# Performance work log

Hardware: AMD Instinct MI355X
Metric: run time of the kernel (lower is better)

## Reference

```python
import jax, jax.numpy as jnp
import numpy as np

PROJ_DIM = 8192
INPUT_DIM = 512
THRESH = 1e-08


def _signed_sqrt(x):
    return jnp.sign(x) * jnp.sqrt(jnp.abs(x))


def _make_sketch_matrix(key, input_dim, proj_dim):
    kh, ks = jax.random.split(key)
    h = jax.random.randint(kh, (input_dim,), 0, proj_dim)
    s = jnp.sign(jax.random.uniform(ks, (input_dim,), minval=-1.0, maxval=1.0)).astype(jnp.float32)
    M = jnp.zeros((input_dim, proj_dim), dtype=jnp.float32)
    return M.at[jnp.arange(input_dim), h].set(s)


def setup_inputs() -> dict:
    key = jax.random.key(0)
    kx, k1, k2 = jax.random.split(key, 3)
    x = jax.random.normal(kx, (32, 14, 14, INPUT_DIM), dtype=jnp.float32)
    M1 = _make_sketch_matrix(k1, INPUT_DIM, PROJ_DIM)
    M2 = _make_sketch_matrix(k2, INPUT_DIM, PROJ_DIM)
    return {"x": x, "M1": M1, "M2": M2}


def reference(x, M1, M2):
    B, H, W, C = x.shape
    x_flat = x.reshape(-1, C)                      # [B*H*W, C]
    # count-sketch projections (dense matmul, as in the original layer)
    p1 = (x_flat @ M1).astype(jnp.complex64)       # [B*H*W, P]
    p2 = (x_flat @ M2).astype(jnp.complex64)
    # circular convolution via FFT
    sketch = jnp.fft.fft(p1, axis=-1) * jnp.fft.fft(p2, axis=-1)
    y = jnp.real(jnp.fft.ifft(sketch, axis=-1)).astype(jnp.float32)
    y = y.reshape(B, H, W, -1).sum(axis=(1, 2))    # sum-pool over spatial dims -> [B, P]
    y = _signed_sqrt(y)
    # tf.nn.l2_normalize(x, axis=1, epsilon=1e-10)
    inv_norm = jax.lax.rsqrt(jnp.maximum(jnp.sum(y * y, axis=1, keepdims=True), 1e-10))
    return y * inv_norm
```

## Files before the change

kernel.cpp:

```cpp
#include <hip/hip_runtime.h>
#include <math.h>

#define PROJ 8192
#define CDIM 512
#define HWPOS 196
#define NBATCH 32
#define NSLAB 7
#define NSEG 16

typedef __attribute__((ext_vector_type(8))) short   short8;
typedef __attribute__((ext_vector_type(4))) float   f32x4;

__device__ __forceinline__ unsigned short f2bf(float f) {
    unsigned u = __float_as_uint(f);
    u += 0x7fff + ((u >> 16) & 1);
    return (unsigned short)(u >> 16);
}
__device__ __forceinline__ float bf2f(unsigned short h) {
    return __uint_as_float(((unsigned)h) << 16);
}

#define BI_PACK 0x2110002110003210ULL
#define BJ_PACK 0x3323213323213210ULL

__device__ __forceinline__ void seg_entry(int seg, int e,
    const int* __restrict__ h1, const float* __restrict__ s1,
    const int* __restrict__ h2, const float* __restrict__ s2,
    int& bin, int& sg)
{
    const int bi = (int)((BI_PACK >> (seg * 4)) & 15);
    const int bj = (int)((BJ_PACK >> (seg * 4)) & 15);
    const int r = e >> 7, c = e & 127;
    int gi, gj;
    if (seg < 10) { gi = bi * 128 + r; gj = bj * 128 + c; }
    else          { gi = bj * 128 + c; gj = bi * 128 + r; }
    bin = (h1[gi] + h2[gj]) & (PROJ - 1);
    sg  = (int)((__float_as_uint(s1[gi]) ^ __float_as_uint(s2[gj])) >> 31);
}

__global__ __launch_bounds__(256) void extract_kernel(
    const float* __restrict__ M1, const float* __restrict__ M2,
    int* __restrict__ h1, float* __restrict__ s1,
    int* __restrict__ h2, float* __restrict__ s2)
{
    const int row = blockIdx.x;
    const float* M = blockIdx.y ? M2 : M1;
    int*   h = blockIdx.y ? h2 : h1;
    float* s = blockIdx.y ? s2 : s1;
    const float* mrow = M + (size_t)row * PROJ;

    for (int i = threadIdx.x * 4; i < PROJ; i += 256 * 4) {
        float4 v = *(const float4*)(mrow + i);
        if (v.x != 0.0f) { h[row] = i + 0; s[row] = v.x; }
        if (v.y != 0.0f) { h[row] = i + 1; s[row] = v.y; }
        if (v.z != 0.0f) { h[row] = i + 2; s[row] = v.z; }
        if (v.w != 0.0f) { h[row] = i + 3; s[row] = v.w; }
    }
}

__global__ __launch_bounds__(256) void combo_kernel(
    const float* __restrict__ x,
    unsigned short* __restrict__ XThi, unsigned short* __restrict__ XTlo,
    const int* __restrict__ h1, const float* __restrict__ s1,
    const int* __restrict__ h2, const float* __restrict__ s2,
    unsigned* __restrict__ csr)
{
    __shared__ __align__(16) char smem[32 * 513 * 4];
    const int tid = threadIdx.x;

    if (blockIdx.x < 224) {
        float (*xt)[513] = (float(*)[513])smem;
        const int ks = blockIdx.x % NSLAB;
        const int bt = blockIdx.x / NSLAB;
        const float* xb = x + (size_t)bt * HWPOS * CDIM;
        const int k0 = ks * 32;
#pragma unroll
        for (int i = 0; i < 16; ++i) {
            const int idx = i * 1024 + tid * 4;
            const int kr  = idx >> 9;
            const int c   = idx & 511;
            float4 v = make_float4(0.f, 0.f, 0.f, 0.f);
            if (k0 + kr < HWPOS) v = *(const float4*)(xb + (size_t)(k0 + kr) * CDIM + c);
            xt[kr][c+0] = v.x; xt[kr][c+1] = v.y; xt[kr][c+2] = v.z; xt[kr][c+3] = v.w;
        }
        __syncthreads();

        unsigned short* ohi = XThi + ((size_t)bt * NSLAB + ks) * 16384;
        unsigned short* olo = XTlo + ((size_t)bt * NSLAB + ks) * 16384;
#pragma unroll
        for (int i = 0; i < 8; ++i) {
            const int ch   = i * 256 + tid;
            const int c16  = ch & 15;
            const int quad = (ch >> 4) & 3;
            const int cgrp = ch >> 6;
            const int c    = cgrp * 16 + c16;
            short8 vh, vl;
#pragma unroll
            for (int j = 0; j < 8; ++j) {
                float f = xt[quad * 8 + j][c];
                unsigned short h = f2bf(f);
                vh[j] = (short)h;
                vl[j] = (short)f2bf(f - bf2f(h));
            }
            *(short8*)(ohi + ch * 8) = vh;
            *(short8*)(olo + ch * 8) = vl;
        }
    } else {
        unsigned* cnt = (unsigned*)smem;
        unsigned* sc  = (unsigned*)(smem + 32768);
        const int seg = blockIdx.x - 224;

        for (int i = tid; i < PROJ; i += 256) cnt[i] = 0u;
        __syncthreads();
#pragma unroll
        for (int k = 0; k < 64; ++k) {
            const int e = k * 256 + tid;
            int bin, sg;
            seg_entry(seg, e, h1, s1, h2, s2, bin, sg);
            atomicAdd(&cnt[bin], 1u);
        }
        __syncthreads();

        unsigned c[32]; unsigned tot = 0;
#pragma unroll
        for (int i = 0; i < 32; ++i) { c[i] = cnt[tid * 32 + i]; tot += c[i]; }
        sc[tid] = tot;
        __syncthreads();
        for (int off = 1; off < 256; off <<= 1) {
            unsigned v = (tid >= off) ? sc[tid - off] : 0u;
            __syncthreads();
            sc[tid] += v;
            __syncthreads();
        }
        unsigned base = sc[tid] - tot;
#pragma unroll
        for (int i = 0; i < 32; ++i) { unsigned t = c[i]; cnt[tid * 32 + i] = base; base += t; }
        __syncthreads();

        unsigned* cs = csr + (size_t)seg * 16384;
#pragma unroll
        for (int k = 0; k < 64; ++k) {
            const int e = k * 256 + tid;
            int bin, sg;
            seg_entry(seg, e, h1, s1, h2, s2, bin, sg);
            const unsigned pos = atomicAdd(&cnt[bin], 1u);
            cs[pos] = ((unsigned)bin << 15) | ((unsigned)sg << 14) | (unsigned)e;
        }
    }
}

__global__ __launch_bounds__(256) void gramgather_kernel(
    const unsigned short* __restrict__ XThi, const unsigned short* __restrict__ XTlo,
    const unsigned* __restrict__ csr, float* __restrict__ pbins)
{
    const int id  = blockIdx.x;
    const int sub = id >> 3;
    const int tp  = sub & 15;
    const int bat = (id & 7) + 8 * (sub >> 4);
    const int bi = (int)((BI_PACK >> (tp * 4)) & 15);
    const int bj = (int)((BJ_PACK >> (tp * 4)) & 15);

    const int tid  = threadIdx.x;
    const int w    = tid >> 6;
    const int lane = tid & 63;
    const int rowq = w >> 1, colq = w & 1;

    __shared__ __align__(16) unsigned short Sbuf[2][4][4096];

    const int tile = (w < 2) ? bi : bj;
    const unsigned short* srcbase = ((w & 1) ? XTlo : XThi)
                                  + (size_t)bat * NSLAB * 16384 + (size_t)tile * 4096;

    {
        const unsigned short* src = srcbase;
        unsigned short* dst = &Sbuf[0][w][0];
#pragma unroll
        for (int i = 0; i < 8; ++i)
            __builtin_amdgcn_global_load_lds(
                (const __attribute__((address_space(1))) void*)(src + i * 512 + lane * 8),
                (__attribute__((address_space(3))) void*)(dst + i * 512), 16, 0, 0);
    }

    float* page = pbins + ((size_t)bat * NSEG + tp) * PROJ;
    for (int i = tid * 4; i < PROJ; i += 1024)
        *(float4*)(page + i) = make_float4(0.f, 0.f, 0.f, 0.f);

    f32x4 acc[16];
#pragma unroll
    for (int i = 0; i < 16; ++i) { acc[i][0]=0.f; acc[i][1]=0.f; acc[i][2]=0.f; acc[i][3]=0.f; }

    for (int ks = 0; ks < NSLAB; ++ks) {
        __syncthreads();
        const int buf = ks & 1;

        if (ks + 1 < NSLAB) {
            const unsigned short* src = srcbase + (size_t)(ks + 1) * 16384;
            unsigned short* dst = &Sbuf[buf ^ 1][w][0];
#pragma unroll
            for (int i = 0; i < 8; ++i)
                __builtin_amdgcn_global_load_lds(
                    (const __attribute__((address_space(1))) void*)(src + i * 512 + lane * 8),
                    (__attribute__((address_space(3))) void*)(dst + i * 512), 16, 0, 0);
        }

        short8 ah[4], al[4], bh4[4], bl[4];
#pragma unroll
        for (int t = 0; t < 4; ++t) {
            ah[t]  = *(const short8*)&Sbuf[buf][0][(rowq * 4 + t) * 512 + lane * 8];
            al[t]  = *(const short8*)&Sbuf[buf][1][(rowq * 4 + t) * 512 + lane * 8];
            bh4[t] = *(const short8*)&Sbuf[buf][2][(colq * 4 + t) * 512 + lane * 8];
            bl[t]  = *(const short8*)&Sbuf[buf][3][(colq * 4 + t) * 512 + lane * 8];
        }
#pragma unroll
        for (int mt = 0; mt < 4; ++mt)
#pragma unroll
            for (int nt = 0; nt < 4; ++nt) {
                const int idx = mt * 4 + nt;
                acc[idx] = __builtin_amdgcn_mfma_f32_16x16x32_bf16(ah[mt], bh4[nt], acc[idx], 0, 0, 0);
                acc[idx] = __builtin_amdgcn_mfma_f32_16x16x32_bf16(ah[mt], bl[nt],  acc[idx], 0, 0, 0);
                acc[idx] = __builtin_amdgcn_mfma_f32_16x16x32_bf16(al[mt], bh4[nt], acc[idx], 0, 0, 0);
            }
    }

    __syncthreads();
    float* tileL = (float*)Sbuf;
    const int quad = lane >> 4;
#pragma unroll
    for (int mt = 0; mt < 4; ++mt)
#pragma unroll
        for (int reg = 0; reg < 4; ++reg) {
            const int rl = rowq * 64 + mt * 16 + quad * 4 + reg;
#pragma unroll
            for (int nt = 0; nt < 4; ++nt) {
                const int cl = colq * 64 + nt * 16 + (lane & 15);
                tileL[rl * 128 + cl] = acc[mt * 4 + nt][reg];
            }
        }
    __syncthreads();

    const uint4* ce = (const uint4*)(csr + (size_t)tp * 16384 + (size_t)tid * 64);
    uint4 E[16];
#pragma unroll
    for (int i = 0; i < 16; ++i) E[i] = ce[i];

    float a = 0.f;
    unsigned cur = E[0].x >> 15;
    bool first = true;
#pragma unroll
    for (int i = 0; i < 16; ++i) {
#pragma unroll
        for (int j = 0; j < 4; ++j) {
            const unsigned ent = (j == 0) ? E[i].x : (j == 1) ? E[i].y
                               : (j == 2) ? E[i].z : E[i].w;
            const unsigned b = ent >> 15;
            float v = tileL[ent & 0x3FFF];
            v = (ent & 0x4000u) ? -v : v;
            if (b != cur) {
                if (first) { unsafeAtomicAdd(&page[cur], a); first = false; }
                else       { page[cur] = a; }
                cur = b; a = v;
            } else {
                a += v;
            }
        }
    }
    unsafeAtomicAdd(&page[cur], a);
}

__global__ __launch_bounds__(512) void finalize_kernel(
    const float* __restrict__ pbins, float* __restrict__ out)
{
    const int bat = blockIdx.x;
    const int tid = threadIdx.x;
    const float* pb = pbins + (size_t)bat * NSEG * PROJ;

    float4 y0, y1, y2, y3;
    float local = 0.f;

#pragma unroll
    for (int c = 0; c < 4; ++c) {
        const int base = c * 2048 + tid * 4;
        float4 a = make_float4(0.f, 0.f, 0.f, 0.f);
#pragma unroll
        for (int t = 0; t < NSEG; ++t) {
            float4 p = *(const float4*)(pb + (size_t)t * PROJ + base);
            a.x += p.x; a.y += p.y; a.z += p.z; a.w += p.w;
        }
        local += fabsf(a.x) + fabsf(a.y) + fabsf(a.z) + fabsf(a.w);
        float4 sv;
        sv.x = (a.x >= 0.f) ? sqrtf(a.x) : -sqrtf(-a.x);
        sv.y = (a.y >= 0.f) ? sqrtf(a.y) : -sqrtf(-a.y);
        sv.z = (a.z >= 0.f) ? sqrtf(a.z) : -sqrtf(-a.z);
        sv.w = (a.w >= 0.f) ? sqrtf(a.w) : -sqrtf(-a.w);
        if (c == 0) y0 = sv; else if (c == 1) y1 = sv; else if (c == 2) y2 = sv; else y3 = sv;
    }

#pragma unroll
    for (int off = 32; off > 0; off >>= 1) local += __shfl_down(local, off, 64);

    __shared__ float wred[8];
    __shared__ float sinv;
    if ((tid & 63) == 0) wred[tid >> 6] = local;
    __syncthreads();
    if (tid == 0) {
        float t = 0.f;
#pragma unroll
        for (int i = 0; i < 8; ++i) t += wred[i];
        sinv = rsqrtf(fmaxf(t, 1e-10f));
    }
    __syncthreads();
    const float inv = sinv;

    float* ob = out + (size_t)bat * PROJ;
#pragma unroll
    for (int c = 0; c < 4; ++c) {
        float4 sv = (c == 0) ? y0 : (c == 1) ? y1 : (c == 2) ? y2 : y3;
        sv.x *= inv; sv.y *= inv; sv.z *= inv; sv.w *= inv;
        *(float4*)(ob + c * 2048 + tid * 4) = sv;
    }
}

extern "C" void kernel_launch(void* const* d_in, const int* in_sizes, int n_in,
                              void* d_out, int out_size, void* d_ws, size_t ws_size,
                              hipStream_t stream)
{
    const float* x  = (const float*)d_in[0];
    const float* M1 = (const float*)d_in[1];
    const float* M2 = (const float*)d_in[2];
    float* out = (float*)d_out;

    char* ws = (char*)d_ws;
    int*            h1    = (int*)   (ws + 0);
    float*          s1    = (float*) (ws + 2048);
    int*            h2    = (int*)   (ws + 4096);
    float*          s2    = (float*) (ws + 6144);
    unsigned*       csr   = (unsigned*)(ws + 16384);
    unsigned short* XThi  = (unsigned short*)(ws + 1064960);
    unsigned short* XTlo  = (unsigned short*)(ws + 8404992);
    float*          pbins = (float*) (ws + 15745024);

    extract_kernel<<<dim3(512, 2), 256, 0, stream>>>(M1, M2, h1, s1, h2, s2);
    combo_kernel<<<240, 256, 0, stream>>>(x, XThi, XTlo, h1, s1, h2, s2, csr);
    gramgather_kernel<<<NSEG * NBATCH, 256, 0, stream>>>(XThi, XTlo, csr, pbins);
    finalize_kernel<<<NBATCH, 512, 0, stream>>>(pbins, out);
}
```

Measured before the change: 179.6 us.

## Split finalize into parallel reduce plus normalize; use raw LDS atomics

New measurement: 162.2 us. 9.7% less time.

```diff
diff --git a/kernel.cpp b/kernel.cpp
--- a/kernel.cpp
+++ b/kernel.cpp
@@ -18,6 +18,20 @@
 }
 __device__ __forceinline__ float bf2f(unsigned short h) {
     return __uint_as_float(((unsigned)h) << 16);
+}
+
+__device__ __forceinline__ void lds_uadd(unsigned* p, unsigned v) {
+    __attribute__((address_space(3))) unsigned* lp =
+        (__attribute__((address_space(3))) unsigned*)p;
+    asm volatile("ds_add_u32 %0, %1" : : "v"(lp), "v"(v) : "memory");
+}
+__device__ __forceinline__ unsigned lds_uadd_rtn(unsigned* p, unsigned v) {
+    __attribute__((address_space(3))) unsigned* lp =
+        (__attribute__((address_space(3))) unsigned*)p;
+    unsigned r;
+    asm volatile("ds_add_rtn_u32 %0, %1, %2\n\ts_waitcnt lgkmcnt(0)"
+                 : "=v"(r) : "v"(lp), "v"(v) : "memory");
+    return r;
 }
 
 #define BI_PACK 0x2110002110003210ULL
@@ -41,13 +55,17 @@
 __global__ __launch_bounds__(256) void extract_kernel(
     const float* __restrict__ M1, const float* __restrict__ M2,
     int* __restrict__ h1, float* __restrict__ s1,
-    int* __restrict__ h2, float* __restrict__ s2)
+    int* __restrict__ h2, float* __restrict__ s2,
+    float* __restrict__ norm)
 {
     const int row = blockIdx.x;
     const float* M = blockIdx.y ? M2 : M1;
     int*   h = blockIdx.y ? h2 : h1;
     float* s = blockIdx.y ? s2 : s1;
     const float* mrow = M + (size_t)row * PROJ;
+
+    if (blockIdx.x == 0 && blockIdx.y == 0 && threadIdx.x < NBATCH)
+        norm[threadIdx.x] = 0.0f;
 
     for (int i = threadIdx.x * 4; i < PROJ; i += 256 * 4) {
         float4 v = *(const float4*)(mrow + i);
@@ -65,11 +83,12 @@
     const int* __restrict__ h2, const float* __restrict__ s2,
     unsigned* __restrict__ csr)
 {
-    __shared__ __align__(16) char smem[32 * 513 * 4];
+    __shared__ float    xt[32][513];
+    __shared__ unsigned cnt[PROJ];
+    __shared__ unsigned sc[256];
     const int tid = threadIdx.x;
 
     if (blockIdx.x < 224) {
-        float (*xt)[513] = (float(*)[513])smem;
         const int ks = blockIdx.x % NSLAB;
         const int bt = blockIdx.x / NSLAB;
         const float* xb = x + (size_t)bt * HWPOS * CDIM;
@@ -106,18 +125,16 @@
             *(short8*)(olo + ch * 8) = vl;
         }
     } else {
-        unsigned* cnt = (unsigned*)smem;
-        unsigned* sc  = (unsigned*)(smem + 32768);
         const int seg = blockIdx.x - 224;
 
         for (int i = tid; i < PROJ; i += 256) cnt[i] = 0u;
         __syncthreads();
-#pragma unroll
+#pragma unroll 8
         for (int k = 0; k < 64; ++k) {
             const int e = k * 256 + tid;
             int bin, sg;
             seg_entry(seg, e, h1, s1, h2, s2, bin, sg);
-            atomicAdd(&cnt[bin], 1u);
+            lds_uadd(&cnt[bin], 1u);
         }
         __syncthreads();
 
@@ -138,12 +155,12 @@
         __syncthreads();
 
         unsigned* cs = csr + (size_t)seg * 16384;
-#pragma unroll
+#pragma unroll 8
         for (int k = 0; k < 64; ++k) {
             const int e = k * 256 + tid;
             int bin, sg;
             seg_entry(seg, e, h1, s1, h2, s2, bin, sg);
-            const unsigned pos = atomicAdd(&cnt[bin], 1u);
+            const unsigned pos = lds_uadd_rtn(&cnt[bin], 1u);
             cs[pos] = ((unsigned)bin << 15) | ((unsigned)sg << 14) | (unsigned)e;
         }
     }
@@ -267,57 +284,51 @@
     unsafeAtomicAdd(&page[cur], a);
 }
 
-__global__ __launch_bounds__(512) void finalize_kernel(
-    const float* __restrict__ pbins, float* __restrict__ out)
-{
-    const int bat = blockIdx.x;
-    const int tid = threadIdx.x;
+__global__ __launch_bounds__(256) void reduce_kernel(
+    const float* __restrict__ pbins, float* __restrict__ out,
+    float* __restrict__ norm)
+{
+    const int chunk = blockIdx.x;
+    const int bat   = blockIdx.y;
+    const int tid   = threadIdx.x;
+    const int base  = chunk * 1024 + tid * 4;
+
     const float* pb = pbins + (size_t)bat * NSEG * PROJ;
-
-    float4 y0, y1, y2, y3;
-    float local = 0.f;
-
-#pragma unroll
-    for (int c = 0; c < 4; ++c) {
-        const int base = c * 2048 + tid * 4;
-        float4 a = make_float4(0.f, 0.f, 0.f, 0.f);
-#pragma unroll
-        for (int t = 0; t < NSEG; ++t) {
-            float4 p = *(const float4*)(pb + (size_t)t * PROJ + base);
-            a.x += p.x; a.y += p.y; a.z += p.z; a.w += p.w;
-        }
-        local += fabsf(a.x) + fabsf(a.y) + fabsf(a.z) + fabsf(a.w);
-        float4 sv;
-        sv.x = (a.x >= 0.f) ? sqrtf(a.x) : -sqrtf(-a.x);
-        sv.y = (a.y >= 0.f) ? sqrtf(a.y) : -sqrtf(-a.y);
-        sv.z = (a.z >= 0.f) ? sqrtf(a.z) : -sqrtf(-a.z);
-        sv.w = (a.w >= 0.f) ? sqrtf(a.w) : -sqrtf(-a.w);
-        if (c == 0) y0 = sv; else if (c == 1) y1 = sv; else if (c == 2) y2 = sv; else y3 = sv;
-    }
-
+    float4 v = make_float4(0.f, 0.f, 0.f, 0.f);
+#pragma unroll
+    for (int t = 0; t < NSEG; ++t) {
+        float4 p = *(const float4*)(pb + (size_t)t * PROJ + base);
+        v.x += p.x; v.y += p.y; v.z += p.z; v.w += p.w;
+    }
+
+    float4 sv;
+    sv.x = (v.x >= 0.f) ? sqrtf(v.x) : -sqrtf(-v.x);
+    sv.y = (v.y >= 0.f) ? sqrtf(v.y) : -sqrtf(-v.y);
+    sv.z = (v.z >= 0.f) ? sqrtf(v.z) : -sqrtf(-v.z);
+    sv.w = (v.w >= 0.f) ? sqrtf(v.w) : -sqrtf(-v.w);
+    *(float4*)(out + (size_t)bat * PROJ + base) = sv;
+
+    float local = fabsf(v.x) + fabsf(v.y) + fabsf(v.z) + fabsf(v.w);
 #pragma unroll
     for (int off = 32; off > 0; off >>= 1) local += __shfl_down(local, off, 64);
 
-    __shared__ float wred[8];
-    __shared__ float sinv;
+    __shared__ float wred[4];
     if ((tid & 63) == 0) wred[tid >> 6] = local;
     __syncthreads();
-    if (tid == 0) {
-        float t = 0.f;
-#pragma unroll
-        for (int i = 0; i < 8; ++i) t += wred[i];
-        sinv = rsqrtf(fmaxf(t, 1e-10f));
-    }
-    __syncthreads();
-    const float inv = sinv;
-
-    float* ob = out + (size_t)bat * PROJ;
-#pragma unroll
-    for (int c = 0; c < 4; ++c) {
-        float4 sv = (c == 0) ? y0 : (c == 1) ? y1 : (c == 2) ? y2 : y3;
-        sv.x *= inv; sv.y *= inv; sv.z *= inv; sv.w *= inv;
-        *(float4*)(ob + c * 2048 + tid * 4) = sv;
-    }
+    if (tid == 0)
+        unsafeAtomicAdd(&norm[bat], wred[0] + wred[1] + wred[2] + wred[3]);
+}
+
+__global__ __launch_bounds__(256) void normalize_kernel(
+    float* __restrict__ out, const float* __restrict__ norm)
+{
+    const int bat = blockIdx.y;
+    const int idx = blockIdx.x * 1024 + threadIdx.x * 4;
+    const float inv = rsqrtf(fmaxf(norm[bat], 1e-10f));
+    float4* p = (float4*)(out + (size_t)bat * PROJ + idx);
+    float4 v = *p;
+    v.x *= inv; v.y *= inv; v.z *= inv; v.w *= inv;
+    *p = v;
 }
 
 extern "C" void kernel_launch(void* const* d_in, const int* in_sizes, int n_in,
@@ -334,13 +345,15 @@
     float*          s1    = (float*) (ws + 2048);
     int*            h2    = (int*)   (ws + 4096);
     float*          s2    = (float*) (ws + 6144);
+    float*          norm  = (float*) (ws + 8192);
     unsigned*       csr   = (unsigned*)(ws + 16384);
     unsigned short* XThi  = (unsigned short*)(ws + 1064960);
     unsigned short* XTlo  = (unsigned short*)(ws + 8404992);
     float*          pbins = (float*) (ws + 15745024);
 
-    extract_kernel<<<dim3(512, 2), 256, 0, stream>>>(M1, M2, h1, s1, h2, s2);
+    extract_kernel<<<dim3(512, 2), 256, 0, stream>>>(M1, M2, h1, s1, h2, s2, norm);
     combo_kernel<<<240, 256, 0, stream>>>(x, XThi, XTlo, h1, s1, h2, s2, csr);
     gramgather_kernel<<<NSEG * NBATCH, 256, 0, stream>>>(XThi, XTlo, csr, pbins);
-    finalize_kernel<<<NBATCH, 512, 0, stream>>>(pbins, out);
-}
+    reduce_kernel<<<dim3(8, NBATCH), 256, 0, stream>>>(pbins, out, norm);
+    normalize_kernel<<<dim3(8, NBATCH), 256, 0, stream>>>(out, norm);
+}
```

## Fuse extract with x transpose, split CSR build, move pbins zeroing earlier

Applied to the files above, without the earlier changes.

Result: no change. 178.2 us (-0.8%).

```diff
diff --git a/kernel.cpp b/kernel.cpp
--- a/kernel.cpp
+++ b/kernel.cpp
@@ -18,6 +18,20 @@
 }
 __device__ __forceinline__ float bf2f(unsigned short h) {
     return __uint_as_float(((unsigned)h) << 16);
+}
+
+__device__ __forceinline__ void lds_uadd(unsigned* p, unsigned v) {
+    __attribute__((address_space(3))) unsigned* lp =
+        (__attribute__((address_space(3))) unsigned*)p;
+    asm volatile("ds_add_u32 %0, %1" : : "v"(lp), "v"(v) : "memory");
+}
+__device__ __forceinline__ unsigned lds_uadd_rtn(unsigned* p, unsigned v) {
+    __attribute__((address_space(3))) unsigned* lp =
+        (__attribute__((address_space(3))) unsigned*)p;
+    unsigned r;
+    asm volatile("ds_add_rtn_u32 %0, %1, %2\n\ts_waitcnt lgkmcnt(0)"
+                 : "=v"(r) : "v"(lp), "v"(v) : "memory");
+    return r;
 }
 
 #define BI_PACK 0x2110002110003210ULL
@@ -38,40 +52,41 @@
     sg  = (int)((__float_as_uint(s1[gi]) ^ __float_as_uint(s2[gj])) >> 31);
 }
 
-__global__ __launch_bounds__(256) void extract_kernel(
+__global__ __launch_bounds__(256) void prep_extract_kernel(
+    const float* __restrict__ x,
     const float* __restrict__ M1, const float* __restrict__ M2,
     int* __restrict__ h1, float* __restrict__ s1,
-    int* __restrict__ h2, float* __restrict__ s2)
-{
-    const int row = blockIdx.x;
-    const float* M = blockIdx.y ? M2 : M1;
-    int*   h = blockIdx.y ? h2 : h1;
-    float* s = blockIdx.y ? s2 : s1;
-    const float* mrow = M + (size_t)row * PROJ;
-
-    for (int i = threadIdx.x * 4; i < PROJ; i += 256 * 4) {
-        float4 v = *(const float4*)(mrow + i);
-        if (v.x != 0.0f) { h[row] = i + 0; s[row] = v.x; }
-        if (v.y != 0.0f) { h[row] = i + 1; s[row] = v.y; }
-        if (v.z != 0.0f) { h[row] = i + 2; s[row] = v.z; }
-        if (v.w != 0.0f) { h[row] = i + 3; s[row] = v.w; }
-    }
-}
-
-__global__ __launch_bounds__(256) void combo_kernel(
-    const float* __restrict__ x,
+    int* __restrict__ h2, float* __restrict__ s2,
     unsigned short* __restrict__ XThi, unsigned short* __restrict__ XTlo,
-    const int* __restrict__ h1, const float* __restrict__ s1,
-    const int* __restrict__ h2, const float* __restrict__ s2,
-    unsigned* __restrict__ csr)
-{
-    __shared__ __align__(16) char smem[32 * 513 * 4];
+    float* __restrict__ pbins)
+{
+    __shared__ float xt[32][513];
+    const int bid = blockIdx.x;
     const int tid = threadIdx.x;
 
-    if (blockIdx.x < 224) {
-        float (*xt)[513] = (float(*)[513])smem;
-        const int ks = blockIdx.x % NSLAB;
-        const int bt = blockIdx.x / NSLAB;
+    if (bid < 1024) {
+        const int row = bid >> 1;
+        const float* M = (bid & 1) ? M2 : M1;
+        int*   h = (bid & 1) ? h2 : h1;
+        float* s = (bid & 1) ? s2 : s1;
+        const float* mrow = M + (size_t)row * PROJ;
+
+        for (int i = tid * 4; i < PROJ; i += 256 * 4) {
+            float4 v = *(const float4*)(mrow + i);
+            if (v.x != 0.0f) { h[row] = i + 0; s[row] = v.x; }
+            if (v.y != 0.0f) { h[row] = i + 1; s[row] = v.y; }
+            if (v.z != 0.0f) { h[row] = i + 2; s[row] = v.z; }
+            if (v.w != 0.0f) { h[row] = i + 3; s[row] = v.w; }
+        }
+
+        float* pz = pbins + (size_t)bid * 4096;
+#pragma unroll
+        for (int i = 0; i < 4; ++i)
+            *(float4*)(pz + i * 1024 + tid * 4) = make_float4(0.f, 0.f, 0.f, 0.f);
+    } else {
+        const int pb = bid - 1024;
+        const int ks = pb % NSLAB;
+        const int bt = pb / NSLAB;
         const float* xb = x + (size_t)bt * HWPOS * CDIM;
         const int k0 = ks * 32;
 #pragma unroll
@@ -105,47 +120,54 @@
             *(short8*)(ohi + ch * 8) = vh;
             *(short8*)(olo + ch * 8) = vl;
         }
-    } else {
-        unsigned* cnt = (unsigned*)smem;
-        unsigned* sc  = (unsigned*)(smem + 32768);
-        const int seg = blockIdx.x - 224;
-
-        for (int i = tid; i < PROJ; i += 256) cnt[i] = 0u;
+    }
+}
+
+__global__ __launch_bounds__(256) void build_kernel(
+    const int* __restrict__ h1, const float* __restrict__ s1,
+    const int* __restrict__ h2, const float* __restrict__ s2,
+    unsigned* __restrict__ csr)
+{
+    __shared__ unsigned cnt[PROJ];
+    __shared__ unsigned sc[256];
+    const int tid = threadIdx.x;
+    const int seg = blockIdx.x;
+
+    for (int i = tid; i < PROJ; i += 256) cnt[i] = 0u;
+    __syncthreads();
+#pragma unroll 8
+    for (int k = 0; k < 64; ++k) {
+        const int e = k * 256 + tid;
+        int bin, sg;
+        seg_entry(seg, e, h1, s1, h2, s2, bin, sg);
+        lds_uadd(&cnt[bin], 1u);
+    }
+    __syncthreads();
+
+    unsigned c[32]; unsigned tot = 0;
+#pragma unroll
+    for (int i = 0; i < 32; ++i) { c[i] = cnt[tid * 32 + i]; tot += c[i]; }
+    sc[tid] = tot;
+    __syncthreads();
+    for (int off = 1; off < 256; off <<= 1) {
+        unsigned v = (tid >= off) ? sc[tid - off] : 0u;
         __syncthreads();
-#pragma unroll
-        for (int k = 0; k < 64; ++k) {
-            const int e = k * 256 + tid;
-            int bin, sg;
-            seg_entry(seg, e, h1, s1, h2, s2, bin, sg);
-            atomicAdd(&cnt[bin], 1u);
-        }
+        sc[tid] += v;
         __syncthreads();
-
-        unsigned c[32]; unsigned tot = 0;
-#pragma unroll
-        for (int i = 0; i < 32; ++i) { c[i] = cnt[tid * 32 + i]; tot += c[i]; }
-        sc[tid] = tot;
-        __syncthreads();
-        for (int off = 1; off < 256; off <<= 1) {
-            unsigned v = (tid >= off) ? sc[tid - off] : 0u;
-            __syncthreads();
-            sc[tid] += v;
-            __syncthreads();
-        }
-        unsigned base = sc[tid] - tot;
-#pragma unroll
-        for (int i = 0; i < 32; ++i) { unsigned t = c[i]; cnt[tid * 32 + i] = base; base += t; }
-        __syncthreads();
-
-        unsigned* cs = csr + (size_t)seg * 16384;
-#pragma unroll
-        for (int k = 0; k < 64; ++k) {
-            const int e = k * 256 + tid;
-            int bin, sg;
-            seg_entry(seg, e, h1, s1, h2, s2, bin, sg);
-            const unsigned pos = atomicAdd(&cnt[bin], 1u);
-            cs[pos] = ((unsigned)bin << 15) | ((unsigned)sg << 14) | (unsigned)e;
-        }
+    }
+    unsigned base = sc[tid] - tot;
+#pragma unroll
+    for (int i = 0; i < 32; ++i) { unsigned t = c[i]; cnt[tid * 32 + i] = base; base += t; }
+    __syncthreads();
+
+    unsigned* cs = csr + (size_t)seg * 16384;
+#pragma unroll 8
+    for (int k = 0; k < 64; ++k) {
+        const int e = k * 256 + tid;
+        int bin, sg;
+        seg_entry(seg, e, h1, s1, h2, s2, bin, sg);
+        const unsigned pos = lds_uadd_rtn(&cnt[bin], 1u);
+        cs[pos] = ((unsigned)bin << 15) | ((unsigned)sg << 14) | (unsigned)e;
     }
 }
 
@@ -182,8 +204,6 @@
     }
 
     float* page = pbins + ((size_t)bat * NSEG + tp) * PROJ;
-    for (int i = tid * 4; i < PROJ; i += 1024)
-        *(float4*)(page + i) = make_float4(0.f, 0.f, 0.f, 0.f);
 
     f32x4 acc[16];
 #pragma unroll
@@ -267,19 +287,19 @@
     unsafeAtomicAdd(&page[cur], a);
 }
 
-__global__ __launch_bounds__(512) void finalize_kernel(
+__global__ __launch_bounds__(1024) void finalize_kernel(
     const float* __restrict__ pbins, float* __restrict__ out)
 {
     const int bat = blockIdx.x;
     const int tid = threadIdx.x;
     const float* pb = pbins + (size_t)bat * NSEG * PROJ;
 
-    float4 y0, y1, y2, y3;
+    float4 y0, y1;
     float local = 0.f;
 
 #pragma unroll
-    for (int c = 0; c < 4; ++c) {
-        const int base = c * 2048 + tid * 4;
+    for (int c = 0; c < 2; ++c) {
+        const int base = c * 4096 + tid * 4;
         float4 a = make_float4(0.f, 0.f, 0.f, 0.f);
 #pragma unroll
         for (int t = 0; t < NSEG; ++t) {
@@ -292,32 +312,30 @@
         sv.y = (a.y >= 0.f) ? sqrtf(a.y) : -sqrtf(-a.y);
         sv.z = (a.z >= 0.f) ? sqrtf(a.z) : -sqrtf(-a.z);
         sv.w = (a.w >= 0.f) ? sqrtf(a.w) : -sqrtf(-a.w);
-        if (c == 0) y0 = sv; else if (c == 1) y1 = sv; else if (c == 2) y2 = sv; else y3 = sv;
+        if (c == 0) y0 = sv; else y1 = sv;
     }
 
 #pragma unroll
     for (int off = 32; off > 0; off >>= 1) local += __shfl_down(local, off, 64);
 
-    __shared__ float wred[8];
+    __shared__ float wred[16];
     __shared__ float sinv;
     if ((tid & 63) == 0) wred[tid >> 6] = local;
     __syncthreads();
     if (tid == 0) {
         float t = 0.f;
 #pragma unroll
-        for (int i = 0; i < 8; ++i) t += wred[i];
+        for (int i = 0; i < 16; ++i) t += wred[i];
         sinv = rsqrtf(fmaxf(t, 1e-10f));
     }
     __syncthreads();
     const float inv = sinv;
 
     float* ob = out + (size_t)bat * PROJ;
-#pragma unroll
-    for (int c = 0; c < 4; ++c) {
-        float4 sv = (c == 0) ? y0 : (c == 1) ? y1 : (c == 2) ? y2 : y3;
-        sv.x *= inv; sv.y *= inv; sv.z *= inv; sv.w *= inv;
-        *(float4*)(ob + c * 2048 + tid * 4) = sv;
-    }
+    y0.x *= inv; y0.y *= inv; y0.z *= inv; y0.w *= inv;
+    y1.x *= inv; y1.y *= inv; y1.z *= inv; y1.w *= inv;
+    *(float4*)(ob + tid * 4)        = y0;
+    *(float4*)(ob + 4096 + tid * 4) = y1;
 }
 
 extern "C" void kernel_launch(void* const* d_in, const int* in_sizes, int n_in,
@@ -339,8 +357,9 @@
     unsigned short* XTlo  = (unsigned short*)(ws + 8404992);
     float*          pbins = (float*) (ws + 15745024);
 
-    extract_kernel<<<dim3(512, 2), 256, 0, stream>>>(M1, M2, h1, s1, h2, s2);
-    combo_kernel<<<240, 256, 0, stream>>>(x, XThi, XTlo, h1, s1, h2, s2, csr);
+    prep_extract_kernel<<<1248, 256, 0, stream>>>(x, M1, M2, h1, s1, h2, s2,
+                                                  XThi, XTlo, pbins);
+    build_kernel<<<NSEG, 256, 0, stream>>>(h1, s1, h2, s2, csr);
     gramgather_kernel<<<NSEG * NBATCH, 256, 0, stream>>>(XThi, XTlo, csr, pbins);
-    finalize_kernel<<<NBATCH, 512, 0, stream>>>(pbins, out);
-}
+    finalize_kernel<<<NBATCH, 1024, 0, stream>>>(pbins, out);
+}
```
